# Kernel optimization log

Measured on AMD Instinct MI355X. Metric: run time of the kernel, lower is better.

## Reference

```python
import jax, jax.numpy as jnp
import numpy as np

NUM_EXPERTS = 8
IN_FEATURES = 2048
OUT_FEATURES = 2048
TOTAL_TOKENS = 16384


def setup_inputs() -> dict:
    key = jax.random.key(0)
    kx, kc, kw, kb = jax.random.split(key, 4)
    X = jax.random.normal(kx, (TOTAL_TOKENS, IN_FEATURES), dtype=jnp.float32)
    # expert_offset: [E+1] monotonically increasing segment boundaries,
    # offset[0] = 0, offset[E] = TOTAL_TOKENS (tokens pre-sorted by expert).
    cuts = jnp.sort(jax.random.randint(kc, (NUM_EXPERTS - 1,), 0, TOTAL_TOKENS))
    expert_offset = jnp.concatenate([
        jnp.zeros((1,), dtype=jnp.int64),
        cuts.astype(jnp.int64),
        jnp.full((1,), TOTAL_TOKENS, dtype=jnp.int64),
    ])
    weight = jax.random.normal(kw, (NUM_EXPERTS, OUT_FEATURES, IN_FEATURES), dtype=jnp.float32) * 0.02
    bias = jax.random.normal(kb, (NUM_EXPERTS, OUT_FEATURES), dtype=jnp.float32) * 0.02
    return {"X": X, "expert_offset": expert_offset, "weight": weight, "bias": bias}


def reference(X, expert_offset, weight, bias):
    # X: [T, in], weight: [E, out, in], bias: [E, out]
    T = X.shape[0]
    E = weight.shape[0]
    # token t belongs to expert e iff offset[e] <= t < offset[e+1]
    eid = jnp.searchsorted(expert_offset[1:], jnp.arange(T), side="right")  # [T]
    Y = bias[eid]  # [T, out] per-token expert bias
    # grouped GEMM expressed as E masked dense GEMMs (E is a small fixed constant)
    for e in range(E):
        mask = (eid == e).astype(X.dtype)[:, None]  # [T, 1]
        Y = Y + mask * (X @ weight[e].T)
    return Y
```

## Files before the change

kernel.cpp:

```cpp
#include <hip/hip_runtime.h>


typedef __attribute__((ext_vector_type(8))) short s16x8;
typedef __attribute__((ext_vector_type(4))) short s16x4;
typedef __attribute__((ext_vector_type(4))) float f32x4;

typedef __attribute__((address_space(1))) void gv_t;
typedef __attribute__((address_space(3))) void lv_t;

#define PBM 256
#define PBN 128
#define PBK 32
#define PTHREADS 512
#define ASLOT (PBM * PBK)
#define BSLOT (PBN * PBK)

#define FBM 128
#define FBN 128
#define FBK 32
#define LDK 40

__device__ __forceinline__ short f2bf(float f) {
    union { float f; unsigned u; } v; v.f = f;
    unsigned r = v.u + 0x7FFFu + ((v.u >> 16) & 1u);
    return (short)(r >> 16);
}

__device__ __forceinline__ long long load_off(const void* p, int i, bool i64) {
    if (i64) return ((const long long*)p)[i];
    return (long long)((const int*)p)[i];
}

__global__ __launch_bounds__(256)
void cvt_kernel(const float* __restrict__ src, short* __restrict__ dst, int n4) {
    int i = blockIdx.x * 256 + threadIdx.x;
    if (i >= n4) return;
    float4 v = ((const float4*)src)[i];
    s16x4 b;
    b.x = f2bf(v.x); b.y = f2bf(v.y); b.z = f2bf(v.z); b.w = f2bf(v.w);
    ((s16x4*)dst)[i] = b;
}

__device__ __forceinline__ bool sched_tile(const void* offp, bool off_i64, int NEXP,
                                           int slot, int bm,
                                           int& e_out, long long& row0, int& rows) {
    int acc_t = 0;
    for (int e = 0; e < NEXP; ++e) {
        long long s = load_off(offp, e, off_i64);
        long long t = load_off(offp, e + 1, off_i64);
        int n = (int)(t - s);
        int nt = (n + bm - 1) / bm;
        if (slot < acc_t + nt) {
            int lt = slot - acc_t;
            row0 = s + (long long)lt * bm;
            rows = (int)(t - row0);
            if (rows > bm) rows = bm;
            e_out = e;
            return true;
        }
        acc_t += nt;
    }
    return false;
}

__global__ __launch_bounds__(PTHREADS, 2)
void moe_gemm_bf16_pipe(const short* __restrict__ Xb16,
                        const void* __restrict__ offp,
                        const short* __restrict__ Wb16,
                        const float* __restrict__ Bias,
                        float* __restrict__ Y,
                        int IN_F, int OUT_F, int NEXP, int Ttot) {
    const bool off_i64 = (((const int*)offp)[NEXP] != Ttot);

    int e_found; long long row0; int rows;
    if (!sched_tile(offp, off_i64, NEXP, blockIdx.y, PBM, e_found, row0, rows)) return;

    const int n0 = blockIdx.x * PBN;
    const int tid = threadIdx.x;
    const int wave = tid >> 6;
    const int lane = tid & 63;
    const int wm = (wave >> 1) * 64;
    const int wn = (wave & 1) * 64;
    const int lrow = lane & 15;
    const int kg = lane >> 4;
    const int sw = (lrow >> 1) & 3;

    __shared__ __align__(16) short As[4 * ASLOT];
    __shared__ __align__(16) short Bs[4 * BSLOT];

    const short* Xb = Xb16 + (size_t)row0 * IN_F;
    const short* Wb = Wb16 + (size_t)e_found * OUT_F * IN_F + (size_t)n0 * IN_F;

    const int lr4 = lane >> 2;
    const int colOff = ((lane & 3) ^ ((lr4 >> 1) & 3)) * 8;
    const int ra0 = wave * 16 + lr4;
    const int ra1 = 128 + wave * 16 + lr4;
    const int ra0c = ra0 < rows ? ra0 : rows - 1;
    const int ra1c = ra1 < rows ? ra1 : rows - 1;
    const int rb = wave * 16 + lr4;

    const short* srcA0 = Xb + (size_t)ra0c * IN_F + colOff;
    const short* srcA1 = Xb + (size_t)ra1c * IN_F + colOff;
    const short* srcB  = Wb + (size_t)rb * IN_F + colOff;
    const int dA0 = wave * 512;
    const int dA1 = (8 + wave) * 512;
    const int dB  = wave * 512;

    const int nkt = IN_F / PBK;

    auto STAGE = [&](int kt_) {
        const int s_ = kt_ & 3;
        const int ko_ = kt_ * PBK;
        __builtin_amdgcn_global_load_lds((gv_t*)(srcA0 + ko_),
                                         (lv_t*)(As + s_ * ASLOT + dA0), 16, 0, 0);
        __builtin_amdgcn_global_load_lds((gv_t*)(srcA1 + ko_),
                                         (lv_t*)(As + s_ * ASLOT + dA1), 16, 0, 0);
        __builtin_amdgcn_global_load_lds((gv_t*)(srcB + ko_),
                                         (lv_t*)(Bs + s_ * BSLOT + dB), 16, 0, 0);
    };

    STAGE(0);
    if (nkt > 1) STAGE(1);
    if (nkt > 2) STAGE(2);

    f32x4 acc[4][4] = {};

    for (int kt = 0; kt < nkt; ++kt) {
        if (kt + 2 < nkt)      asm volatile("s_waitcnt vmcnt(6)" ::: "memory");
        else if (kt + 1 < nkt) asm volatile("s_waitcnt vmcnt(3)" ::: "memory");
        else                   asm volatile("s_waitcnt vmcnt(0)" ::: "memory");
        asm volatile("s_barrier" ::: "memory");

        if (kt + 3 < nkt) STAGE(kt + 3);

        const short* aS = As + (kt & 3) * ASLOT;
        const short* bS = Bs + (kt & 3) * BSLOT;
        s16x8 af[4], bf[4];
        #pragma unroll
        for (int i = 0; i < 4; ++i)
            af[i] = *(const s16x8*)&aS[(wm + i * 16 + lrow) * PBK + ((kg ^ sw) * 8)];
        #pragma unroll
        for (int j = 0; j < 4; ++j)
            bf[j] = *(const s16x8*)&bS[(wn + j * 16 + lrow) * PBK + ((kg ^ sw) * 8)];

        __builtin_amdgcn_s_setprio(1);
        #pragma unroll
        for (int i = 0; i < 4; ++i)
            #pragma unroll
            for (int j = 0; j < 4; ++j)
                acc[i][j] = __builtin_amdgcn_mfma_f32_16x16x32_bf16(
                    af[i], bf[j], acc[i][j], 0, 0, 0);
        __builtin_amdgcn_s_setprio(0);
    }

    float bv[4];
    #pragma unroll
    for (int j = 0; j < 4; ++j)
        bv[j] = Bias[(size_t)e_found * OUT_F + n0 + wn + j * 16 + lrow];

    #pragma unroll
    for (int i = 0; i < 4; ++i) {
        #pragma unroll
        for (int r = 0; r < 4; ++r) {
            int rr = wm + i * 16 + kg * 4 + r;
            if (rr < rows) {
                float* yrow = Y + (size_t)(row0 + rr) * OUT_F + n0;
                #pragma unroll
                for (int j = 0; j < 4; ++j)
                    yrow[wn + j * 16 + lrow] = acc[i][j][r] + bv[j];
            }
        }
    }
}

__global__ __launch_bounds__(256, 2)
void moe_gemm_f32(const float* __restrict__ X,
                  const void* __restrict__ offp,
                  const float* __restrict__ W,
                  const float* __restrict__ Bias,
                  float* __restrict__ Y,
                  int IN_F, int OUT_F, int NEXP, int Ttot) {
    const bool off_i64 = (((const int*)offp)[NEXP] != Ttot);
    int e_found; long long row0; int rows;
    if (!sched_tile(offp, off_i64, NEXP, blockIdx.y, FBM, e_found, row0, rows)) return;

    const int n0 = blockIdx.x * FBN;
    const int tid = threadIdx.x;
    const int wave = tid >> 6;
    const int lane = tid & 63;
    const int wm = (wave & 1) * 64;
    const int wn = (wave >> 1) * 64;
    const int lrow = lane & 15;
    const int kg = lane >> 4;

    __shared__ __align__(16) short As[FBM][LDK];
    __shared__ __align__(16) short Bs[FBN][LDK];

    const float* Xb = X + (size_t)row0 * IN_F;
    const float* Wb = W + (size_t)e_found * OUT_F * IN_F + (size_t)n0 * IN_F;

    f32x4 acc[4][4] = {};

    for (int k0 = 0; k0 < IN_F; k0 += FBK) {
        __syncthreads();
        #pragma unroll
        for (int p = 0; p < 4; ++p) {
            int idx = p * 256 + tid;
            int r = idx >> 3;
            int kc = (idx & 7) << 2;
            float4 v = make_float4(0.f, 0.f, 0.f, 0.f);
            if (r < rows) v = *(const float4*)(Xb + (size_t)r * IN_F + k0 + kc);
            s16x4 b;
            b.x = f2bf(v.x); b.y = f2bf(v.y); b.z = f2bf(v.z); b.w = f2bf(v.w);
            *(s16x4*)&As[r][kc] = b;
        }
        #pragma unroll
        for (int p = 0; p < 4; ++p) {
            int idx = p * 256 + tid;
            int r = idx >> 3;
            int kc = (idx & 7) << 2;
            float4 v = *(const float4*)(Wb + (size_t)r * IN_F + k0 + kc);
            s16x4 b;
            b.x = f2bf(v.x); b.y = f2bf(v.y); b.z = f2bf(v.z); b.w = f2bf(v.w);
            *(s16x4*)&Bs[r][kc] = b;
        }
        __syncthreads();

        s16x8 af[4], bf[4];
        #pragma unroll
        for (int i = 0; i < 4; ++i)
            af[i] = *(const s16x8*)&As[wm + i * 16 + lrow][kg * 8];
        #pragma unroll
        for (int j = 0; j < 4; ++j)
            bf[j] = *(const s16x8*)&Bs[wn + j * 16 + lrow][kg * 8];

        #pragma unroll
        for (int i = 0; i < 4; ++i)
            #pragma unroll
            for (int j = 0; j < 4; ++j)
                acc[i][j] = __builtin_amdgcn_mfma_f32_16x16x32_bf16(
                    af[i], bf[j], acc[i][j], 0, 0, 0);
    }

    float bv[4];
    #pragma unroll
    for (int j = 0; j < 4; ++j)
        bv[j] = Bias[(size_t)e_found * OUT_F + n0 + wn + j * 16 + lrow];

    #pragma unroll
    for (int i = 0; i < 4; ++i) {
        #pragma unroll
        for (int r = 0; r < 4; ++r) {
            int rr = wm + i * 16 + kg * 4 + r;
            if (rr < rows) {
                float* yrow = Y + (size_t)(row0 + rr) * OUT_F + n0;
                #pragma unroll
                for (int j = 0; j < 4; ++j)
                    yrow[wn + j * 16 + lrow] = acc[i][j][r] + bv[j];
            }
        }
    }
}

extern "C" void kernel_launch(void* const* d_in, const int* in_sizes, int n_in,
                              void* d_out, int out_size, void* d_ws, size_t ws_size,
                              hipStream_t stream) {
    const float* X = (const float*)d_in[0];
    const void* off = d_in[1];
    const float* W = (const float*)d_in[2];
    const float* Bias = (const float*)d_in[3];
    float* Y = (float*)d_out;

    const int NEXP1 = in_sizes[1];
    const int NEXP = NEXP1 - 1;
    const int OUT_F = in_sizes[3] / NEXP;
    const int IN_F = (int)((long long)in_sizes[2] / NEXP / OUT_F);
    const int T = in_sizes[0] / IN_F;

    const long long Xn = (long long)T * IN_F;
    const long long Wn = (long long)NEXP * OUT_F * IN_F;
    const size_t need = (size_t)(Xn + Wn) * sizeof(short);

    const bool shape_ok = (OUT_F % PBN == 0) && (IN_F % PBK == 0) &&
                          (Xn % 4 == 0) && (Wn % 4 == 0);

    if (shape_ok && ws_size >= need) {
        short* wsX = (short*)d_ws;
        short* wsW = wsX + Xn;
        {
            int n4 = (int)(Xn / 4);
            cvt_kernel<<<(n4 + 255) / 256, 256, 0, stream>>>(X, wsX, n4);
        }
        {
            int n4 = (int)(Wn / 4);
            cvt_kernel<<<(n4 + 255) / 256, 256, 0, stream>>>(W, wsW, n4);
        }
        const int maxRowTiles = T / PBM + NEXP;
        dim3 grid(OUT_F / PBN, maxRowTiles);
        moe_gemm_bf16_pipe<<<grid, PTHREADS, 0, stream>>>(wsX, off, wsW, Bias, Y,
                                                          IN_F, OUT_F, NEXP, T);
    } else {
        const int maxRowTiles = T / FBM + NEXP;
        dim3 grid(OUT_F / FBN, maxRowTiles);
        moe_gemm_f32<<<grid, 256, 0, stream>>>(X, off, W, Bias, Y,
                                               IN_F, OUT_F, NEXP, T);
    }
}
```

Measured before the change: 613.2 us.

## Replace pipelined 256x128 GEMM with single-buffer 128x128 tiles and XCD-aware remap

Drops the 4-stage LDS pipeline with 512-thread 256x128 tiles and uses 256-thread 128x128 tiles with a single LDS buffer and two barriers per k-step. Adds a workgroup-index remap that spreads tiles across the eight XCDs, and turns the bf16 conversion into a grid-stride kernel that writes 8 elements per thread. The aim is smaller blocks, lower LDS use and better L2 locality per XCD, but global-load latency is no longer overlapped with MFMA work and setprio is removed.

Result: faster. 529.5 us (-13.6%).

```diff
diff --git a/kernel.cpp b/kernel.cpp
--- a/kernel.cpp
+++ b/kernel.cpp
@@ -8,12 +8,9 @@
 typedef __attribute__((address_space(1))) void gv_t;
 typedef __attribute__((address_space(3))) void lv_t;
 
-#define PBM 256
-#define PBN 128
-#define PBK 32
-#define PTHREADS 512
-#define ASLOT (PBM * PBK)
-#define BSLOT (PBN * PBK)
+#define BM 128
+#define BN 128
+#define BK 32
 
 #define FBM 128
 #define FBN 128
@@ -32,13 +29,16 @@
 }
 
 __global__ __launch_bounds__(256)
-void cvt_kernel(const float* __restrict__ src, short* __restrict__ dst, int n4) {
-    int i = blockIdx.x * 256 + threadIdx.x;
-    if (i >= n4) return;
-    float4 v = ((const float4*)src)[i];
-    s16x4 b;
-    b.x = f2bf(v.x); b.y = f2bf(v.y); b.z = f2bf(v.z); b.w = f2bf(v.w);
-    ((s16x4*)dst)[i] = b;
+void cvt_kernel(const float* __restrict__ src, short* __restrict__ dst, long long n8) {
+    long long stride = (long long)gridDim.x * 256;
+    for (long long i = (long long)blockIdx.x * 256 + threadIdx.x; i < n8; i += stride) {
+        float4 a = ((const float4*)src)[2 * i];
+        float4 b = ((const float4*)src)[2 * i + 1];
+        s16x8 o;
+        o[0] = f2bf(a.x); o[1] = f2bf(a.y); o[2] = f2bf(a.z); o[3] = f2bf(a.w);
+        o[4] = f2bf(b.x); o[5] = f2bf(b.y); o[6] = f2bf(b.z); o[7] = f2bf(b.w);
+        ((s16x8*)dst)[i] = o;
+    }
 }
 
 __device__ __forceinline__ bool sched_tile(const void* offp, bool off_i64, int NEXP,
@@ -63,94 +63,84 @@
     return false;
 }
 
-__global__ __launch_bounds__(PTHREADS, 2)
-void moe_gemm_bf16_pipe(const short* __restrict__ Xb16,
-                        const void* __restrict__ offp,
-                        const short* __restrict__ Wb16,
-                        const float* __restrict__ Bias,
-                        float* __restrict__ Y,
-                        int IN_F, int OUT_F, int NEXP, int Ttot) {
+__global__ __launch_bounds__(256)
+void moe_gemm_bf16(const short* __restrict__ Xb16,
+                   const void* __restrict__ offp,
+                   const short* __restrict__ Wb16,
+                   const float* __restrict__ Bias,
+                   float* __restrict__ Y,
+                   int IN_F, int OUT_F, int NEXP, int Ttot) {
     const bool off_i64 = (((const int*)offp)[NEXP] != Ttot);
 
+    const int gx = gridDim.x, gy = gridDim.y;
+    const int nwg = gx * gy;
+    const int hw = blockIdx.x + gx * blockIdx.y;
+    const int q = nwg >> 3, r = nwg & 7;
+    const int xcd = hw & 7, lid = hw >> 3;
+    const int work = (xcd < r ? xcd * (q + 1) : r * (q + 1) + (xcd - r) * q) + lid;
+    const int wx = work / gy;
+    const int wy = work % gy;
+
     int e_found; long long row0; int rows;
-    if (!sched_tile(offp, off_i64, NEXP, blockIdx.y, PBM, e_found, row0, rows)) return;
-
-    const int n0 = blockIdx.x * PBN;
+    if (!sched_tile(offp, off_i64, NEXP, wy, BM, e_found, row0, rows)) return;
+
+    const int n0 = wx * BN;
     const int tid = threadIdx.x;
     const int wave = tid >> 6;
     const int lane = tid & 63;
-    const int wm = (wave >> 1) * 64;
-    const int wn = (wave & 1) * 64;
+    const int wm = (wave & 1) * 64;
+    const int wn = (wave >> 1) * 64;
     const int lrow = lane & 15;
     const int kg = lane >> 4;
-    const int sw = (lrow >> 1) & 3;
-
-    __shared__ __align__(16) short As[4 * ASLOT];
-    __shared__ __align__(16) short Bs[4 * BSLOT];
+    const int swr = (lrow >> 1) & 3;
+
+    __shared__ __align__(16) short As[BM * BK];
+    __shared__ __align__(16) short Bs[BN * BK];
 
     const short* Xb = Xb16 + (size_t)row0 * IN_F;
     const short* Wb = Wb16 + (size_t)e_found * OUT_F * IN_F + (size_t)n0 * IN_F;
 
     const int lr4 = lane >> 2;
     const int colOff = ((lane & 3) ^ ((lr4 >> 1) & 3)) * 8;
-    const int ra0 = wave * 16 + lr4;
-    const int ra1 = 128 + wave * 16 + lr4;
+    const int rbase = wave * 16 + lr4;
+    const int ra0 = rbase;
+    const int ra1 = 64 + rbase;
     const int ra0c = ra0 < rows ? ra0 : rows - 1;
     const int ra1c = ra1 < rows ? ra1 : rows - 1;
-    const int rb = wave * 16 + lr4;
 
     const short* srcA0 = Xb + (size_t)ra0c * IN_F + colOff;
     const short* srcA1 = Xb + (size_t)ra1c * IN_F + colOff;
-    const short* srcB  = Wb + (size_t)rb * IN_F + colOff;
+    const short* srcB0 = Wb + (size_t)rbase * IN_F + colOff;
+    const short* srcB1 = Wb + (size_t)(64 + rbase) * IN_F + colOff;
     const int dA0 = wave * 512;
-    const int dA1 = (8 + wave) * 512;
-    const int dB  = wave * 512;
-
-    const int nkt = IN_F / PBK;
-
-    auto STAGE = [&](int kt_) {
-        const int s_ = kt_ & 3;
-        const int ko_ = kt_ * PBK;
-        __builtin_amdgcn_global_load_lds((gv_t*)(srcA0 + ko_),
-                                         (lv_t*)(As + s_ * ASLOT + dA0), 16, 0, 0);
-        __builtin_amdgcn_global_load_lds((gv_t*)(srcA1 + ko_),
-                                         (lv_t*)(As + s_ * ASLOT + dA1), 16, 0, 0);
-        __builtin_amdgcn_global_load_lds((gv_t*)(srcB + ko_),
-                                         (lv_t*)(Bs + s_ * BSLOT + dB), 16, 0, 0);
-    };
-
-    STAGE(0);
-    if (nkt > 1) STAGE(1);
-    if (nkt > 2) STAGE(2);
+    const int dA1 = 2048 + wave * 512;
+    const int dB0 = wave * 512;
+    const int dB1 = 2048 + wave * 512;
 
     f32x4 acc[4][4] = {};
 
-    for (int kt = 0; kt < nkt; ++kt) {
-        if (kt + 2 < nkt)      asm volatile("s_waitcnt vmcnt(6)" ::: "memory");
-        else if (kt + 1 < nkt) asm volatile("s_waitcnt vmcnt(3)" ::: "memory");
-        else                   asm volatile("s_waitcnt vmcnt(0)" ::: "memory");
-        asm volatile("s_barrier" ::: "memory");
-
-        if (kt + 3 < nkt) STAGE(kt + 3);
-
-        const short* aS = As + (kt & 3) * ASLOT;
-        const short* bS = Bs + (kt & 3) * BSLOT;
+    for (int k0 = 0; k0 < IN_F; k0 += BK) {
+        __syncthreads();
+        __builtin_amdgcn_global_load_lds((gv_t*)(srcA0 + k0), (lv_t*)(As + dA0), 16, 0, 0);
+        __builtin_amdgcn_global_load_lds((gv_t*)(srcA1 + k0), (lv_t*)(As + dA1), 16, 0, 0);
+        __builtin_amdgcn_global_load_lds((gv_t*)(srcB0 + k0), (lv_t*)(Bs + dB0), 16, 0, 0);
+        __builtin_amdgcn_global_load_lds((gv_t*)(srcB1 + k0), (lv_t*)(Bs + dB1), 16, 0, 0);
+        __syncthreads();
+
         s16x8 af[4], bf[4];
         #pragma unroll
         for (int i = 0; i < 4; ++i)
-            af[i] = *(const s16x8*)&aS[(wm + i * 16 + lrow) * PBK + ((kg ^ sw) * 8)];
+            af[i] = *(const s16x8*)&As[(wm + i * 16 + lrow) * BK + ((kg ^ swr) * 8)];
         #pragma unroll
         for (int j = 0; j < 4; ++j)
-            bf[j] = *(const s16x8*)&bS[(wn + j * 16 + lrow) * PBK + ((kg ^ sw) * 8)];
-
-        __builtin_amdgcn_s_setprio(1);
+            bf[j] = *(const s16x8*)&Bs[(wn + j * 16 + lrow) * BK + ((kg ^ swr) * 8)];
+
         #pragma unroll
         for (int i = 0; i < 4; ++i)
             #pragma unroll
             for (int j = 0; j < 4; ++j)
                 acc[i][j] = __builtin_amdgcn_mfma_f32_16x16x32_bf16(
                     af[i], bf[j], acc[i][j], 0, 0, 0);
-        __builtin_amdgcn_s_setprio(0);
     }
 
     float bv[4];
@@ -161,13 +151,13 @@
     #pragma unroll
     for (int i = 0; i < 4; ++i) {
         #pragma unroll
-        for (int r = 0; r < 4; ++r) {
-            int rr = wm + i * 16 + kg * 4 + r;
+        for (int r2 = 0; r2 < 4; ++r2) {
+            int rr = wm + i * 16 + kg * 4 + r2;
             if (rr < rows) {
                 float* yrow = Y + (size_t)(row0 + rr) * OUT_F + n0;
                 #pragma unroll
                 for (int j = 0; j < 4; ++j)
-                    yrow[wn + j * 16 + lrow] = acc[i][j][r] + bv[j];
+                    yrow[wn + j * 16 + lrow] = acc[i][j][r2] + bv[j];
             }
         }
     }
@@ -250,13 +240,13 @@
     #pragma unroll
     for (int i = 0; i < 4; ++i) {
         #pragma unroll
-        for (int r = 0; r < 4; ++r) {
-            int rr = wm + i * 16 + kg * 4 + r;
+        for (int r2 = 0; r2 < 4; ++r2) {
+            int rr = wm + i * 16 + kg * 4 + r2;
             if (rr < rows) {
                 float* yrow = Y + (size_t)(row0 + rr) * OUT_F + n0;
                 #pragma unroll
                 for (int j = 0; j < 4; ++j)
-                    yrow[wn + j * 16 + lrow] = acc[i][j][r] + bv[j];
+                    yrow[wn + j * 16 + lrow] = acc[i][j][r2] + bv[j];
             }
         }
     }
@@ -281,24 +271,26 @@
     const long long Wn = (long long)NEXP * OUT_F * IN_F;
     const size_t need = (size_t)(Xn + Wn) * sizeof(short);
 
-    const bool shape_ok = (OUT_F % PBN == 0) && (IN_F % PBK == 0) &&
-                          (Xn % 4 == 0) && (Wn % 4 == 0);
+    const bool shape_ok = (OUT_F % BN == 0) && (IN_F % BK == 0) &&
+                          (Xn % 8 == 0) && (Wn % 8 == 0);
 
     if (shape_ok && ws_size >= need) {
         short* wsX = (short*)d_ws;
         short* wsW = wsX + Xn;
         {
-            int n4 = (int)(Xn / 4);
-            cvt_kernel<<<(n4 + 255) / 256, 256, 0, stream>>>(X, wsX, n4);
+            long long n8 = Xn / 8;
+            int blks = (int)((n8 + 255) / 256); if (blks > 2048) blks = 2048;
+            cvt_kernel<<<blks, 256, 0, stream>>>(X, wsX, n8);
         }
         {
-            int n4 = (int)(Wn / 4);
-            cvt_kernel<<<(n4 + 255) / 256, 256, 0, stream>>>(W, wsW, n4);
-        }
-        const int maxRowTiles = T / PBM + NEXP;
-        dim3 grid(OUT_F / PBN, maxRowTiles);
-        moe_gemm_bf16_pipe<<<grid, PTHREADS, 0, stream>>>(wsX, off, wsW, Bias, Y,
-                                                          IN_F, OUT_F, NEXP, T);
+            long long n8 = Wn / 8;
+            int blks = (int)((n8 + 255) / 256); if (blks > 2048) blks = 2048;
+            cvt_kernel<<<blks, 256, 0, stream>>>(W, wsW, n8);
+        }
+        const int maxRowTiles = T / BM + NEXP;
+        dim3 grid(OUT_F / BN, maxRowTiles);
+        moe_gemm_bf16<<<grid, 256, 0, stream>>>(wsX, off, wsW, Bias, Y,
+                                                IN_F, OUT_F, NEXP, T);
     } else {
         const int maxRowTiles = T / FBM + NEXP;
         dim3 grid(OUT_F / FBN, maxRowTiles);
```
